# Kernel optimization log

Hardware: AMD Instinct MI355X
Metric: run time of the kernel (lower is better)

## Reference

```python
import jax, jax.numpy as jnp
import numpy as np

E, C, K, S = 8, 128, 512, 512  # embedding_dim, channels, kernel_size, stride
NEG_SLOPE = 0.01  # torch F.leaky_relu default


def setup_inputs() -> dict:
    key = jax.random.key(0)
    ks = jax.random.split(key, 11)
    B, T = 4, 1_000_000
    sc = 0.05
    return {
        "x": jax.random.normal(ks[0], (B, T, E), jnp.float32),
        # ctx_conv: Conv1d(E, 2C, K, stride=S) -> weight (2C, E, K), bias (2C,)
        "ctx_conv_w": jax.random.normal(ks[1], (2 * C, E, K), jnp.float32) * sc,
        "ctx_conv_b": jax.random.normal(ks[2], (2 * C,), jnp.float32) * sc,
        # ctx_share: Conv1d(C, C, 1) -> (C, C) pointwise
        "ctx_share_w": jax.random.normal(ks[3], (C, C), jnp.float32) * sc,
        "ctx_share_b": jax.random.normal(ks[4], (C,), jnp.float32) * sc,
        "main_conv_w": jax.random.normal(ks[5], (2 * C, E, K), jnp.float32) * sc,
        "main_conv_b": jax.random.normal(ks[6], (2 * C,), jnp.float32) * sc,
        "main_share_w": jax.random.normal(ks[7], (C, C), jnp.float32) * sc,
        "main_share_b": jax.random.normal(ks[8], (C,), jnp.float32) * sc,
        # gct_proj: Linear(C, C) -> weight (C, C) (y = g @ W.T + b)
        "gct_proj_w": jax.random.normal(ks[9], (C, C), jnp.float32) * sc,
        "gct_proj_b": jax.random.normal(ks[10], (C,), jnp.float32) * sc,
    }


def _leaky(x):
    return jnp.where(x >= 0, x, NEG_SLOPE * x)


def _glu(x):  # GLU over channel dim 1
    a, b = jnp.split(x, 2, axis=1)
    return a * jax.nn.sigmoid(b)


def _conv(z, w, b):
    # z: (B, Cin, T), w: (Cout, Cin, K) -> (B, Cout, T_out), stride S, VALID
    y = jax.lax.conv_general_dilated(z, w, (S,), 'VALID',
                                     dimension_numbers=('NCH', 'OIH', 'NCH'))
    return y + b[None, :, None]


def _branch_act(z, wc, bc, ws, bs):
    # glu(conv(z)) -> leaky_relu(1x1 share conv)
    h = _glu(_conv(z, wc, bc))                                   # (B, C, T_out)
    h = _leaky(jnp.einsum('oc,bct->bot', ws, h) + bs[None, :, None])
    return h


def reference(x, ctx_conv_w, ctx_conv_b, ctx_share_w, ctx_share_b,
              main_conv_w, main_conv_b, main_share_w, main_share_b,
              gct_proj_w, gct_proj_b):
    z = jnp.transpose(x, (0, 2, 1))  # (B, E, T)
    # Context branch: global max over time of ctx activations (GCG context).
    g = _branch_act(z, ctx_conv_w, ctx_conv_b, ctx_share_w, ctx_share_b)
    gct = jnp.max(g, axis=-1)  # (B, C)
    # Main branch with global channel gating.
    h = _branch_act(z, main_conv_w, main_conv_b, main_share_w, main_share_b)  # (B, C, T_out)
    q = jnp.tanh(gct @ gct_proj_w.T + gct_proj_b)                # (B, C)
    gate = jax.nn.sigmoid(jnp.einsum('bct,bc->bt', h, q))        # (B, T_out)
    out = jnp.max(h * gate[:, None, :], axis=-1)                 # (B, C)
    return out
```

## Files before the change

### kernel.cpp

```cpp
#include <hip/hip_runtime.h>
#include <hip/hip_bf16.h>
#include <cmath>

#define B_    4
#define T_    1000000
#define E_    8
#define C_    128
#define NCH   512
#define KK    4096
#define TOUT  1953
#define TP    1956
#define NT2   31

typedef __attribute__((ext_vector_type(8))) short bf16x8;
typedef __attribute__((ext_vector_type(4))) float f32x4;

__device__ __forceinline__ float sigmoidf_(float v) { return 1.f / (1.f + __expf(-v)); }

__device__ __forceinline__ void gload_lds16(const void* g, void* l) {
  __builtin_amdgcn_global_load_lds(
      (const __attribute__((address_space(1))) void*)g,
      (__attribute__((address_space(3))) void*)l, 16, 0, 0);
}

__global__ __launch_bounds__(256) void prep_inputs(
    const float* __restrict__ wc, const float* __restrict__ bc,
    const float* __restrict__ wm, const float* __restrict__ bm,
    __hip_bfloat16* __restrict__ Wn2, float* __restrict__ bias_t) {
  __shared__ float row[KK];
  const int n = blockIdx.x, br = n >> 8, o = n & 255;
  const float* wsrc = (br ? wm : wc) + (size_t)o * KK;
  for (int i = threadIdx.x; i < KK; i += 256) row[i] = wsrc[i];
  __syncthreads();
  const int nt = n >> 4, nr = n & 15;
  for (int k = threadIdx.x; k < KK; k += 256) {
    int kpos = k >> 3, e = k & 7;
    size_t addr = (((size_t)nt * 128 + (k >> 5)) * 64
                   + (size_t)((k >> 3) & 3) * 16 + nr) * 8 + (k & 7);
    Wn2[addr] = __float2bfloat16(row[e * 512 + kpos]);
  }
  if (threadIdx.x == 0) bias_t[n] = (br ? bm : bc)[o];
}

__global__ __launch_bounds__(512, 2) void mfma_gemm(
    const float* __restrict__ x, const __hip_bfloat16* __restrict__ Wn2,
    float* __restrict__ u2) {
  __shared__ float Aldf[2][8192];
  __shared__ __hip_bfloat16 Bs[2][8192];

  const int tid  = threadIdx.x;
  const int lane = tid & 63, wave = tid >> 6;
  const int wt = wave & 3, wn = wave >> 2;

  const int L   = blockIdx.x;
  const int xcd = L & 7;
  const int r   = L >> 3;
  const int nb  = r & 3;
  const int sh  = r >> 2;
  const int s   = sh * 8 + xcd;
  const int tblk = s & 15, b = s >> 4;
  const int t0 = tblk * 128, n0 = nb * 128;

  const float* pAsrc[4];
  int dstA[4];
#pragma unroll
  for (int q = 0; q < 4; ++q) {
    int m  = wave * 4 + q;
    int rl = m * 4 + (lane >> 4);
    int u  = (lane & 15) ^ (rl & 7);
    int rt = t0 + rl;
    if (rt >= TOUT) rt = 0;
    pAsrc[q] = x + (size_t)b * 8000000ull + (size_t)rt * KK + u * 4;
    dstA[q]  = m * 256;
  }
  const __hip_bfloat16* gB = Wn2 + ((size_t)(nb * 8 + wave) * 128) * 512
                             + (size_t)lane * 8;

  f32x4 acc[2][4];
#pragma unroll
  for (int i = 0; i < 2; ++i)
#pragma unroll
    for (int j = 0; j < 4; ++j) acc[i][j] = (f32x4)(0.0f);

  auto STAGE = [&](int buf, int step) {
#pragma unroll
    for (int q = 0; q < 4; ++q)
      gload_lds16(pAsrc[q] + (size_t)step * 64, &Aldf[buf][dstA[q]]);
    const __hip_bfloat16* g = gB + (size_t)step * 1024;
    gload_lds16(g,       &Bs[buf][(size_t)(wave * 2) * 512]);
    gload_lds16(g + 512, &Bs[buf][(size_t)(wave * 2 + 1) * 512]);
  };

  auto COMPUTE = [&](int buf) {
    const int lnlo = lane & 15;
    const int pb = ((lane >> 4) * 2) ^ (lnlo & 7);
    bf16x8 aF[2][2], bF[4][2];
#pragma unroll
    for (int i = 0; i < 2; ++i) {
      const int Rb = wt * 32 + i * 16 + lnlo;
#pragma unroll
      for (int c = 0; c < 2; ++c) {
        const float* base = &Aldf[buf][Rb * 64 + c * 32];
        f32x4 q0 = *(const f32x4*)(base + (pb)      * 4);
        f32x4 q1 = *(const f32x4*)(base + (pb ^ 1) * 4);
        union { __hip_bfloat16 h[8]; bf16x8 v; } u_;
        u_.h[0] = __float2bfloat16(q0[0]); u_.h[1] = __float2bfloat16(q0[1]);
        u_.h[2] = __float2bfloat16(q0[2]); u_.h[3] = __float2bfloat16(q0[3]);
        u_.h[4] = __float2bfloat16(q1[0]); u_.h[5] = __float2bfloat16(q1[1]);
        u_.h[6] = __float2bfloat16(q1[2]); u_.h[7] = __float2bfloat16(q1[3]);
        aF[i][c] = u_.v;
      }
    }
#pragma unroll
    for (int j = 0; j < 4; ++j)
#pragma unroll
      for (int c = 0; c < 2; ++c)
        bF[j][c] = *(const bf16x8*)(&Bs[buf][(size_t)((wn * 4 + j) * 2 + c) * 512
                                             + (size_t)lane * 8]);
#pragma unroll
    for (int c = 0; c < 2; ++c)
#pragma unroll
      for (int i = 0; i < 2; ++i)
#pragma unroll
        for (int j = 0; j < 4; ++j)
          acc[i][j] = __builtin_amdgcn_mfma_f32_16x16x32_bf16(aF[i][c], bF[j][c],
                                                              acc[i][j], 0, 0, 0);
  };

  STAGE(0, 0);
  __syncthreads();

  int cur = 0;
#pragma unroll 1
  for (int step = 0; step < 64; ++step) {
    if (step + 1 < 64) STAGE(cur ^ 1, step + 1);
    COMPUTE(cur);
    __syncthreads();
    cur ^= 1;
  }

  const int crow = (lane >> 4) * 4;
  const int ccol = lane & 15;
#pragma unroll
  for (int j = 0; j < 4; ++j) {
    int n = n0 + wn * 64 + j * 16 + ccol;
    float* urow = u2 + ((size_t)n * B_ + b) * TP;
#pragma unroll
    for (int i = 0; i < 2; ++i) {
      int t = t0 + wt * 32 + i * 16 + crow;
      if (t < TOUT) *(f32x4*)(urow + t) = acc[i][j];
    }
  }
}

__global__ __launch_bounds__(256) void share_act(
    const float* __restrict__ u2, const float* __restrict__ bias_t,
    const float* __restrict__ wsc, const float* __restrict__ bsc,
    const float* __restrict__ wsm, const float* __restrict__ bsm,
    float* __restrict__ hmain, float* __restrict__ gct_part) {
  __shared__ float Wl[128 * 132];
  __shared__ float ul[128 * 68];
  const int tid  = threadIdx.x;
  const int tile = blockIdx.x;
  const int b    = blockIdx.y;
  const int br   = blockIdx.z;
  const int t0   = tile * 64;
  const float* ws = br ? wsm : wsc;
  const float* bs = br ? bsm : bsc;

  for (int g = tid; g < 16384; g += 256) {
    int co = g >> 7, cp = g & 127;
    Wl[cp * 132 + co] = ws[g];
  }
  const size_t base_v = ((size_t)(br * 256) * B_ + b) * TP;
  const size_t base_g = ((size_t)(br * 256 + 128) * B_ + b) * TP;
  for (int g = tid; g < 8192; g += 256) {
    int cp = g >> 6, t = g & 63;
    float v = 0.f;
    if (t0 + t < TOUT) {
      float va = u2[base_v + (size_t)cp * B_ * TP + t0 + t] + bias_t[br * 256 + cp];
      float vg = u2[base_g + (size_t)cp * B_ * TP + t0 + t] + bias_t[br * 256 + 128 + cp];
      v = va * sigmoidf_(vg);
    }
    ul[cp * 68 + t] = v;
  }
  __syncthreads();

  const int ty = tid >> 4, tx = tid & 15;
  float acc[8][4];
#pragma unroll
  for (int i = 0; i < 8; ++i)
#pragma unroll
    for (int j = 0; j < 4; ++j) acc[i][j] = 0.f;

  for (int cp = 0; cp < 128; ++cp) {
    float4 a0 = *(const float4*)&Wl[cp*132 + ty*4];
    float4 a1 = *(const float4*)&Wl[cp*132 + 64 + ty*4];
    float4 b4 = *(const float4*)&ul[cp*68 + tx*4];
    float av[8] = {a0.x,a0.y,a0.z,a0.w,a1.x,a1.y,a1.z,a1.w};
    float bv[4] = {b4.x,b4.y,b4.z,b4.w};
#pragma unroll
    for (int i = 0; i < 8; ++i)
#pragma unroll
      for (int j = 0; j < 4; ++j) acc[i][j] = fmaf(av[i], bv[j], acc[i][j]);
  }

  float mloc[8];
#pragma unroll
  for (int i = 0; i < 8; ++i) mloc[i] = -INFINITY;
#pragma unroll
  for (int i = 0; i < 8; ++i) {
    int c = (i < 4) ? (ty*4 + i) : (64 + ty*4 + (i - 4));
    float bias = bs[c];
#pragma unroll
    for (int j = 0; j < 4; ++j) {
      int t = t0 + tx*4 + j;
      if (t >= TOUT) continue;
      float v = acc[i][j] + bias;
      v = (v >= 0.f) ? v : 0.01f * v;
      if (br == 1) {
        hmain[((size_t)b * 128 + c) * TOUT + t] = v;
      } else {
        mloc[i] = fmaxf(mloc[i], v);
      }
    }
  }
  if (br == 0) {
    __syncthreads();
    float* red = ul;
#pragma unroll
    for (int i = 0; i < 8; ++i) {
      int c = (i < 4) ? (ty*4 + i) : (64 + ty*4 + (i - 4));
      red[c * 16 + tx] = mloc[i];
    }
    __syncthreads();
    if (tid < 128) {
      float m = -INFINITY;
#pragma unroll
      for (int k = 0; k < 16; ++k) m = fmaxf(m, red[tid * 16 + k]);
      gct_part[((size_t)b * 128 + tid) * NT2 + tile] = m;
    }
  }
}

__global__ void gct_q(const float* __restrict__ gct_part, const float* __restrict__ wp,
                      const float* __restrict__ bp, float* __restrict__ q) {
  int b = blockIdx.x, tid = threadIdx.x;
  __shared__ float g[128];
  float m = -INFINITY;
  for (int tl = 0; tl < NT2; ++tl) m = fmaxf(m, gct_part[((size_t)b * 128 + tid) * NT2 + tl]);
  g[tid] = m;
  __syncthreads();
  float s = bp[tid];
  for (int c = 0; c < 128; ++c) s = fmaf(g[c], wp[tid * 128 + c], s);
  q[b * 128 + tid] = tanhf(s);
}

__global__ __launch_bounds__(256) void gate_max(
    const float* __restrict__ hmain, const float* __restrict__ q,
    float* __restrict__ out_part) {
  __shared__ float hl[128 * 68];
  __shared__ float ql[128];
  __shared__ float red[256];
  __shared__ float gl[64];
  int tid = threadIdx.x, tile = blockIdx.x, b = blockIdx.y;
  int t0 = tile * 64;
  for (int g = tid; g < 8192; g += 256) {
    int c = g >> 6, t = g & 63;
    hl[c * 68 + t] = (t0 + t < TOUT) ? hmain[((size_t)b * 128 + c) * TOUT + t0 + t] : 0.f;
  }
  if (tid < 128) ql[tid] = q[b * 128 + tid];
  __syncthreads();
  {
    int t = tid & 63, cy = tid >> 6;
    float s = 0.f;
#pragma unroll
    for (int cc = 0; cc < 32; ++cc) s = fmaf(hl[(cy * 32 + cc) * 68 + t], ql[cy * 32 + cc], s);
    red[cy * 64 + t] = s;
  }
  __syncthreads();
  if (tid < 64) {
    float s = red[tid] + red[64 + tid] + red[128 + tid] + red[192 + tid];
    gl[tid] = sigmoidf_(s);
  }
  __syncthreads();
  {
    int c = tid >> 1, th = tid & 1;
    float m = -INFINITY;
#pragma unroll
    for (int tt = 0; tt < 32; ++tt) {
      int t = th * 32 + tt;
      if (t0 + t < TOUT) m = fmaxf(m, hl[c * 68 + t] * gl[t]);
    }
    red[c * 2 + th] = m;
  }
  __syncthreads();
  if (tid < 128) out_part[((size_t)b * 128 + tid) * NT2 + tile] = fmaxf(red[tid * 2], red[tid * 2 + 1]);
}

__global__ void final_max(const float* __restrict__ out_part, float* __restrict__ out) {
  int idx = blockIdx.x * 256 + threadIdx.x;
  if (idx < 512) {
    float m = -INFINITY;
    for (int tl = 0; tl < NT2; ++tl) m = fmaxf(m, out_part[(size_t)idx * NT2 + tl]);
    out[idx] = m;
  }
}

extern "C" void kernel_launch(void* const* d_in, const int* in_sizes, int n_in,
                              void* d_out, int out_size, void* d_ws, size_t ws_size,
                              hipStream_t stream) {
  const float* x      = (const float*)d_in[0];
  const float* ctx_w  = (const float*)d_in[1];
  const float* ctx_b  = (const float*)d_in[2];
  const float* ctx_sw = (const float*)d_in[3];
  const float* ctx_sb = (const float*)d_in[4];
  const float* main_w = (const float*)d_in[5];
  const float* main_b = (const float*)d_in[6];
  const float* main_sw= (const float*)d_in[7];
  const float* main_sb= (const float*)d_in[8];
  const float* gp_w   = (const float*)d_in[9];
  const float* gp_b   = (const float*)d_in[10];

  char* w = (char*)d_ws;
  __hip_bfloat16* Wn2 = (__hip_bfloat16*)(w);
  float* bias_t  = (float*)(w + 4194304);
  float* u2      = (float*)(w + 4196352);
  float* hmain   = (float*)(w + 20219904);
  float* gct_part= (float*)(w + 24219648);
  float* q       = (float*)(w + 24283136);
  float* out_part= (float*)(w + 24285184);

  prep_inputs<<<NCH, 256, 0, stream>>>(ctx_w, ctx_b, main_w, main_b, Wn2, bias_t);
  mfma_gemm<<<256, 512, 0, stream>>>(x, Wn2, u2);
  share_act<<<dim3(NT2, B_, 2), 256, 0, stream>>>(u2, bias_t, ctx_sw, ctx_sb,
                                                  main_sw, main_sb, hmain, gct_part);
  gct_q<<<B_, 128, 0, stream>>>(gct_part, gp_w, gp_b, q);
  gate_max<<<dim3(NT2, B_), 256, 0, stream>>>(hmain, q, out_part);
  final_max<<<2, 256, 0, stream>>>(out_part, (float*)d_out);
}
```

Measured before the change: 340.3 us.

## Split GEMM reduction dimension in two across blocks with partial-sum buffers

The conv GEMM is split-K by 2. The launch grows from 256 to 512 blocks, each half reduces over 2048 of the 4096 K elements into its own partial output buffer, and the LDS tiles are halved. share_act then sums the two partials before bias and GLU. The goal is more parallelism and occupancy (launch bounds raised to 4 blocks per CU) to keep all CUs busy. The cost is an extra partial-sum buffer write and read plus more workspace.

After: 310.9 us. 8.6% less time.

```diff
diff --git a/kernel.cpp b/kernel.cpp
--- a/kernel.cpp
+++ b/kernel.cpp
@@ -42,39 +42,42 @@
   if (threadIdx.x == 0) bias_t[n] = (br ? bm : bc)[o];
 }
 
-__global__ __launch_bounds__(512, 2) void mfma_gemm(
+__global__ __launch_bounds__(512, 4) void mfma_gemm(
     const float* __restrict__ x, const __hip_bfloat16* __restrict__ Wn2,
-    float* __restrict__ u2) {
-  __shared__ float Aldf[2][8192];
-  __shared__ __hip_bfloat16 Bs[2][8192];
+    float* __restrict__ u2a, float* __restrict__ u2b) {
+  __shared__ float Aldf[2][4096];
+  __shared__ __hip_bfloat16 Bs[2][4096];
 
   const int tid  = threadIdx.x;
   const int lane = tid & 63, wave = tid >> 6;
   const int wt = wave & 3, wn = wave >> 2;
 
-  const int L   = blockIdx.x;
-  const int xcd = L & 7;
-  const int r   = L >> 3;
-  const int nb  = r & 3;
-  const int sh  = r >> 2;
-  const int s   = sh * 8 + xcd;
+  const int L    = blockIdx.x;
+  const int xcd  = L & 7;
+  const int r    = L >> 3;
+  const int inner= r & 7;
+  const int nb   = inner >> 1;
+  const int kb   = inner & 1;
+  const int sh   = r >> 3;
+  const int s    = sh * 8 + xcd;
   const int tblk = s & 15, b = s >> 4;
   const int t0 = tblk * 128, n0 = nb * 128;
-
-  const float* pAsrc[4];
-  int dstA[4];
-#pragma unroll
-  for (int q = 0; q < 4; ++q) {
-    int m  = wave * 4 + q;
-    int rl = m * 4 + (lane >> 4);
-    int u  = (lane & 15) ^ (rl & 7);
+  const int kbase = kb * 2048;
+
+  const float* pAsrc[2];
+  int dstA[2];
+#pragma unroll
+  for (int q = 0; q < 2; ++q) {
+    int m  = wave * 2 + q;
+    int rl = m * 8 + (lane >> 3);
+    int u  = (lane & 7) ^ ((lane >> 3) & 7);
     int rt = t0 + rl;
     if (rt >= TOUT) rt = 0;
-    pAsrc[q] = x + (size_t)b * 8000000ull + (size_t)rt * KK + u * 4;
+    pAsrc[q] = x + (size_t)b * 8000000ull + (size_t)rt * KK + kbase + u * 4;
     dstA[q]  = m * 256;
   }
-  const __hip_bfloat16* gB = Wn2 + ((size_t)(nb * 8 + wave) * 128) * 512
-                             + (size_t)lane * 8;
+  const __hip_bfloat16* gB = Wn2
+      + ((size_t)(nb * 8 + wave) * 128 + kb * 64) * 512 + (size_t)lane * 8;
 
   f32x4 acc[2][4];
 #pragma unroll
@@ -84,47 +87,38 @@
 
   auto STAGE = [&](int buf, int step) {
 #pragma unroll
-    for (int q = 0; q < 4; ++q)
-      gload_lds16(pAsrc[q] + (size_t)step * 64, &Aldf[buf][dstA[q]]);
-    const __hip_bfloat16* g = gB + (size_t)step * 1024;
-    gload_lds16(g,       &Bs[buf][(size_t)(wave * 2) * 512]);
-    gload_lds16(g + 512, &Bs[buf][(size_t)(wave * 2 + 1) * 512]);
+    for (int q = 0; q < 2; ++q)
+      gload_lds16(pAsrc[q] + (size_t)step * 32, &Aldf[buf][dstA[q]]);
+    gload_lds16(gB + (size_t)step * 512, &Bs[buf][(size_t)wave * 512]);
   };
 
   auto COMPUTE = [&](int buf) {
     const int lnlo = lane & 15;
-    const int pb = ((lane >> 4) * 2) ^ (lnlo & 7);
-    bf16x8 aF[2][2], bF[4][2];
+    const int p0 = ((lane >> 4) * 2) ^ (lnlo & 7);
+    bf16x8 aF[2], bF[4];
 #pragma unroll
     for (int i = 0; i < 2; ++i) {
       const int Rb = wt * 32 + i * 16 + lnlo;
-#pragma unroll
-      for (int c = 0; c < 2; ++c) {
-        const float* base = &Aldf[buf][Rb * 64 + c * 32];
-        f32x4 q0 = *(const f32x4*)(base + (pb)      * 4);
-        f32x4 q1 = *(const f32x4*)(base + (pb ^ 1) * 4);
-        union { __hip_bfloat16 h[8]; bf16x8 v; } u_;
-        u_.h[0] = __float2bfloat16(q0[0]); u_.h[1] = __float2bfloat16(q0[1]);
-        u_.h[2] = __float2bfloat16(q0[2]); u_.h[3] = __float2bfloat16(q0[3]);
-        u_.h[4] = __float2bfloat16(q1[0]); u_.h[5] = __float2bfloat16(q1[1]);
-        u_.h[6] = __float2bfloat16(q1[2]); u_.h[7] = __float2bfloat16(q1[3]);
-        aF[i][c] = u_.v;
-      }
+      const float* base = &Aldf[buf][Rb * 32];
+      f32x4 q0 = *(const f32x4*)(base + (p0)     * 4);
+      f32x4 q1 = *(const f32x4*)(base + (p0 ^ 1) * 4);
+      union { __hip_bfloat16 h[8]; bf16x8 v; } u_;
+      u_.h[0] = __float2bfloat16(q0[0]); u_.h[1] = __float2bfloat16(q0[1]);
+      u_.h[2] = __float2bfloat16(q0[2]); u_.h[3] = __float2bfloat16(q0[3]);
+      u_.h[4] = __float2bfloat16(q1[0]); u_.h[5] = __float2bfloat16(q1[1]);
+      u_.h[6] = __float2bfloat16(q1[2]); u_.h[7] = __float2bfloat16(q1[3]);
+      aF[i] = u_.v;
     }
 #pragma unroll
     for (int j = 0; j < 4; ++j)
-#pragma unroll
-      for (int c = 0; c < 2; ++c)
-        bF[j][c] = *(const bf16x8*)(&Bs[buf][(size_t)((wn * 4 + j) * 2 + c) * 512
-                                             + (size_t)lane * 8]);
-#pragma unroll
-    for (int c = 0; c < 2; ++c)
-#pragma unroll
-      for (int i = 0; i < 2; ++i)
-#pragma unroll
-        for (int j = 0; j < 4; ++j)
-          acc[i][j] = __builtin_amdgcn_mfma_f32_16x16x32_bf16(aF[i][c], bF[j][c],
-                                                              acc[i][j], 0, 0, 0);
+      bF[j] = *(const bf16x8*)(&Bs[buf][(size_t)(wn * 4 + j) * 512
+                                        + (size_t)lane * 8]);
+#pragma unroll
+    for (int i = 0; i < 2; ++i)
+#pragma unroll
+      for (int j = 0; j < 4; ++j)
+        acc[i][j] = __builtin_amdgcn_mfma_f32_16x16x32_bf16(aF[i], bF[j],
+                                                            acc[i][j], 0, 0, 0);
   };
 
   STAGE(0, 0);
@@ -139,6 +133,7 @@
     cur ^= 1;
   }
 
+  float* u2 = kb ? u2b : u2a;
   const int crow = (lane >> 4) * 4;
   const int ccol = lane & 15;
 #pragma unroll
@@ -154,7 +149,8 @@
 }
 
 __global__ __launch_bounds__(256) void share_act(
-    const float* __restrict__ u2, const float* __restrict__ bias_t,
+    const float* __restrict__ u2a, const float* __restrict__ u2b,
+    const float* __restrict__ bias_t,
     const float* __restrict__ wsc, const float* __restrict__ bsc,
     const float* __restrict__ wsm, const float* __restrict__ bsm,
     float* __restrict__ hmain, float* __restrict__ gct_part) {
@@ -178,8 +174,10 @@
     int cp = g >> 6, t = g & 63;
     float v = 0.f;
     if (t0 + t < TOUT) {
-      float va = u2[base_v + (size_t)cp * B_ * TP + t0 + t] + bias_t[br * 256 + cp];
-      float vg = u2[base_g + (size_t)cp * B_ * TP + t0 + t] + bias_t[br * 256 + 128 + cp];
+      size_t ia = base_v + (size_t)cp * B_ * TP + t0 + t;
+      size_t ig = base_g + (size_t)cp * B_ * TP + t0 + t;
+      float va = u2a[ia] + u2b[ia] + bias_t[br * 256 + cp];
+      float vg = u2a[ig] + u2b[ig] + bias_t[br * 256 + 128 + cp];
       v = va * sigmoidf_(vg);
     }
     ul[cp * 68 + t] = v;
@@ -325,15 +323,16 @@
   char* w = (char*)d_ws;
   __hip_bfloat16* Wn2 = (__hip_bfloat16*)(w);
   float* bias_t  = (float*)(w + 4194304);
-  float* u2      = (float*)(w + 4196352);
-  float* hmain   = (float*)(w + 20219904);
-  float* gct_part= (float*)(w + 24219648);
-  float* q       = (float*)(w + 24283136);
-  float* out_part= (float*)(w + 24285184);
+  float* u2a     = (float*)(w + 4196352);
+  float* u2b     = (float*)(w + 20219904);
+  float* hmain   = (float*)(w + 36243456);
+  float* gct_part= (float*)(w + 40243200);
+  float* q       = (float*)(w + 40306688);
+  float* out_part= (float*)(w + 40308736);
 
   prep_inputs<<<NCH, 256, 0, stream>>>(ctx_w, ctx_b, main_w, main_b, Wn2, bias_t);
-  mfma_gemm<<<256, 512, 0, stream>>>(x, Wn2, u2);
-  share_act<<<dim3(NT2, B_, 2), 256, 0, stream>>>(u2, bias_t, ctx_sw, ctx_sb,
+  mfma_gemm<<<512, 512, 0, stream>>>(x, Wn2, u2a, u2b);
+  share_act<<<dim3(NT2, B_, 2), 256, 0, stream>>>(u2a, u2b, bias_t, ctx_sw, ctx_sb,
                                                   main_sw, main_sb, hmain, gct_part);
   gct_q<<<B_, 128, 0, stream>>>(gct_part, gp_w, gp_b, q);
   gate_max<<<dim3(NT2, B_), 256, 0, stream>>>(hmain, q, out_part);
```
